# Performance work log

Measured on AMD Instinct MI355X. Metric: run time of the kernel, lower is better.

## Reference

```python
import jax, jax.numpy as jnp
import numpy as np

NUM_TABLES = 8
NUM_EMBEDDINGS = 100000
EMBED_DIM = 128
IDS_PER_FEATURE = 200000


def setup_inputs() -> dict:
    key = jax.random.key(0)
    k_ids, k_w = jax.random.split(key)
    values = jax.random.randint(
        k_ids, (NUM_TABLES, IDS_PER_FEATURE), 0, NUM_EMBEDDINGS, dtype=jnp.int64
    )
    bound = np.sqrt(1.0 / NUM_EMBEDDINGS).astype(np.float32)
    weights = jax.random.uniform(
        k_w, (NUM_TABLES, NUM_EMBEDDINGS, EMBED_DIM),
        minval=-bound, maxval=bound, dtype=jnp.float32
    )
    return {"values": values, "weights": weights}


def reference(values, weights):
    # Per-table gather: weights[t][values[t]] -> [T, N, D]
    gathered = jax.vmap(lambda w, v: jnp.take(w, v, axis=0))(weights, values)
    # torch.cat(unpooled_embeddings, dim=0) -> [T*N, D]
    return gathered.reshape(-1, EMBED_DIM)
```

## Files before the change

### kernel.cpp

```cpp
#include <hip/hip_runtime.h>

constexpr int NUM_TABLES = 8;
constexpr int NUM_EMB    = 100000;
constexpr int DIM        = 128;
constexpr int IDS        = 200000;
constexpr int ROWS       = NUM_TABLES * IDS;

typedef float floatx4 __attribute__((ext_vector_type(4)));

__global__ __launch_bounds__(256) void grouped_embedding_gather(
    const int* __restrict__ vals,
    const float* __restrict__ weights,
    float* __restrict__ out) {
  const int lane       = threadIdx.x & 31;
  const int rowInBlock = threadIdx.x >> 5;
  const int rowsPerBlk = blockDim.x >> 5;
  const int rowStride  = gridDim.x * rowsPerBlk;

  for (int r = blockIdx.x * rowsPerBlk + rowInBlock; r < ROWS; r += rowStride) {
    const int id = __builtin_nontemporal_load(vals + r);
    const int t  = r / IDS;
    const floatx4* __restrict__ src = reinterpret_cast<const floatx4*>(
        weights + ((size_t)t * NUM_EMB + (size_t)id) * DIM);
    floatx4 v = src[lane];
    floatx4* dst = reinterpret_cast<floatx4*>(out + (size_t)r * DIM) + lane;
    __builtin_nontemporal_store(v, dst);
  }
}

extern "C" void kernel_launch(void* const* d_in, const int* in_sizes, int n_in,
                              void* d_out, int out_size, void* d_ws, size_t ws_size,
                              hipStream_t stream) {
  const int*   vals    = (const int*)d_in[0];
  const float* weights = (const float*)d_in[1];
  float*       out     = (float*)d_out;

  const int blocks = 2048;
  grouped_embedding_gather<<<blocks, 256, 0, stream>>>(vals, weights, out);
}
```

Baseline: 256.7 us.

## Replace direct gather with counting-sort by row id and multicast stores

Builds a histogram of ids per table, prefix-scans it, and scatters output row indices into buckets so each unique embedding row is read once and written to all of its destinations. The aim is to cut redundant weight reads when ids repeat. In exchange it adds seven kernel launches, global atomics, extra workspace traffic and random-order output stores. The output write volume, which dominates, is unchanged.

```diff
diff --git a/kernel.cpp b/kernel.cpp
--- a/kernel.cpp
+++ b/kernel.cpp
@@ -1,10 +1,13 @@
 #include <hip/hip_runtime.h>
 
-constexpr int NUM_TABLES = 8;
-constexpr int NUM_EMB    = 100000;
-constexpr int DIM        = 128;
-constexpr int IDS        = 200000;
-constexpr int ROWS       = NUM_TABLES * IDS;
+constexpr int T    = 8;
+constexpr int E    = 100000;
+constexpr int D    = 128;
+constexpr int N    = 200000;
+constexpr int ROWS = T * N;
+constexpr int NU   = T * E;
+constexpr int EPB  = 4096;
+constexpr int NBLK = (NU + EPB - 1) / EPB;
 
 typedef float floatx4 __attribute__((ext_vector_type(4)));
 
@@ -16,15 +19,129 @@
   const int rowInBlock = threadIdx.x >> 5;
   const int rowsPerBlk = blockDim.x >> 5;
   const int rowStride  = gridDim.x * rowsPerBlk;
-
   for (int r = blockIdx.x * rowsPerBlk + rowInBlock; r < ROWS; r += rowStride) {
     const int id = __builtin_nontemporal_load(vals + r);
-    const int t  = r / IDS;
-    const floatx4* __restrict__ src = reinterpret_cast<const floatx4*>(
-        weights + ((size_t)t * NUM_EMB + (size_t)id) * DIM);
+    const int t  = r / N;
+    const floatx4* src = reinterpret_cast<const floatx4*>(
+        weights + ((size_t)t * E + (size_t)id) * D);
     floatx4 v = src[lane];
-    floatx4* dst = reinterpret_cast<floatx4*>(out + (size_t)r * DIM) + lane;
-    __builtin_nontemporal_store(v, dst);
+    __builtin_nontemporal_store(
+        v, reinterpret_cast<floatx4*>(out + (size_t)r * D) + lane);
+  }
+}
+
+__global__ __launch_bounds__(256) void k_zero(unsigned* __restrict__ counts) {
+  int i = blockIdx.x * blockDim.x + threadIdx.x;
+  int stride = gridDim.x * blockDim.x;
+  for (; i < NU; i += stride) counts[i] = 0u;
+}
+
+__global__ __launch_bounds__(256) void k_hist(const int* __restrict__ vals,
+                                              unsigned* __restrict__ counts) {
+  int r = blockIdx.x * blockDim.x + threadIdx.x;
+  int stride = gridDim.x * blockDim.x;
+  for (; r < ROWS; r += stride) {
+    int id = __builtin_nontemporal_load(vals + r);
+    atomicAdd(&counts[(r / N) * E + id], 1u);
+  }
+}
+
+__global__ __launch_bounds__(256) void k_reduce(const unsigned* __restrict__ counts,
+                                                unsigned* __restrict__ partials) {
+  __shared__ unsigned s[256];
+  const int base = blockIdx.x * EPB;
+  unsigned sum = 0;
+  for (int k = 0; k < 16; ++k) {
+    int j = base + threadIdx.x + k * 256;
+    if (j < NU) sum += counts[j];
+  }
+  s[threadIdx.x] = sum;
+  __syncthreads();
+  for (int off = 128; off > 0; off >>= 1) {
+    if (threadIdx.x < off) s[threadIdx.x] += s[threadIdx.x + off];
+    __syncthreads();
+  }
+  if (threadIdx.x == 0) partials[blockIdx.x] = s[0];
+}
+
+__global__ void k_scan_partials(unsigned* __restrict__ partials) {
+  if (threadIdx.x == 0 && blockIdx.x == 0) {
+    unsigned acc = 0;
+    for (int i = 0; i < NBLK; ++i) {
+      unsigned v = partials[i];
+      partials[i] = acc;
+      acc += v;
+    }
+  }
+}
+
+__global__ __launch_bounds__(256) void k_apply(const unsigned* __restrict__ counts,
+                                               const unsigned* __restrict__ partials,
+                                               unsigned* __restrict__ offsets,
+                                               unsigned* __restrict__ cursors) {
+  __shared__ unsigned s[256];
+  const int base = blockIdx.x * EPB + threadIdx.x * 16;
+  unsigned loc[16];
+  unsigned tot = 0;
+  for (int k = 0; k < 16; ++k) {
+    int j = base + k;
+    unsigned c = (j < NU) ? counts[j] : 0u;
+    loc[k] = tot;
+    tot += c;
+  }
+  s[threadIdx.x] = tot;
+  __syncthreads();
+  for (int off = 1; off < 256; off <<= 1) {
+    unsigned v = (threadIdx.x >= (unsigned)off) ? s[threadIdx.x - off] : 0u;
+    __syncthreads();
+    s[threadIdx.x] += v;
+    __syncthreads();
+  }
+  const unsigned excl = s[threadIdx.x] - tot;
+  const unsigned blockBase = partials[blockIdx.x];
+  for (int k = 0; k < 16; ++k) {
+    int j = base + k;
+    if (j < NU) {
+      unsigned o = blockBase + excl + loc[k];
+      offsets[j] = o;
+      cursors[j] = o;
+    }
+  }
+}
+
+__global__ __launch_bounds__(256) void k_scatter(const int* __restrict__ vals,
+                                                 unsigned* __restrict__ cursors,
+                                                 unsigned* __restrict__ sorted_r) {
+  int r = blockIdx.x * blockDim.x + threadIdx.x;
+  int stride = gridDim.x * blockDim.x;
+  for (; r < ROWS; r += stride) {
+    int id = __builtin_nontemporal_load(vals + r);
+    unsigned pos = atomicAdd(&cursors[(r / N) * E + id], 1u);
+    sorted_r[pos] = (unsigned)r;
+  }
+}
+
+__global__ __launch_bounds__(256) void k_multicast(
+    const float* __restrict__ weights,
+    const unsigned* __restrict__ counts,
+    const unsigned* __restrict__ offsets,
+    const unsigned* __restrict__ sorted_r,
+    float* __restrict__ out) {
+  const int lane = threadIdx.x & 31;
+  const int grp  = threadIdx.x >> 5;
+  const int gpb  = blockDim.x >> 5;
+  const int ustride = gridDim.x * gpb;
+  for (int u = blockIdx.x * gpb + grp; u < NU; u += ustride) {
+    const unsigned c = counts[u];
+    if (c == 0) continue;
+    const unsigned start = offsets[u];
+    const floatx4 row =
+        reinterpret_cast<const floatx4*>(weights + (size_t)u * D)[lane];
+    for (unsigned k = 0; k < c; ++k) {
+      const unsigned rr = sorted_r[start + k];
+      __builtin_nontemporal_store(
+          row, reinterpret_cast<floatx4*>(out + (size_t)rr * D) + lane);
+    }
   }
 }
 
@@ -35,6 +152,23 @@
   const float* weights = (const float*)d_in[1];
   float*       out     = (float*)d_out;
 
-  const int blocks = 2048;
-  grouped_embedding_gather<<<blocks, 256, 0, stream>>>(vals, weights, out);
+  const size_t need = ((size_t)NU * 3 + 256 + (size_t)ROWS) * sizeof(unsigned);
+  if (ws_size < need) {
+    grouped_embedding_gather<<<2048, 256, 0, stream>>>(vals, weights, out);
+    return;
+  }
+
+  unsigned* counts   = (unsigned*)d_ws;
+  unsigned* offsets  = counts + NU;
+  unsigned* cursors  = offsets + NU;
+  unsigned* partials = cursors + NU;
+  unsigned* sorted_r = partials + 256;
+
+  k_zero<<<1024, 256, 0, stream>>>(counts);
+  k_hist<<<2048, 256, 0, stream>>>(vals, counts);
+  k_reduce<<<NBLK, 256, 0, stream>>>(counts, partials);
+  k_scan_partials<<<1, 64, 0, stream>>>(partials);
+  k_apply<<<NBLK, 256, 0, stream>>>(counts, partials, offsets, cursors);
+  k_scatter<<<2048, 256, 0, stream>>>(vals, cursors, sorted_r);
+  k_multicast<<<2048, 256, 0, stream>>>(weights, counts, offsets, sorted_r, out);
 }
```

Measured after the change: 437.8 us. 70.5% more time.
